# Performance work log

Hardware: AMD Instinct MI355X
Metric: run time of the kernel (lower is better)

## Reference

```python
import jax, jax.numpy as jnp
import numpy as np

B, S, H, D = 4, 2048, 16, 1024  # batch, seq, heads, n_units
DK = D // H


def setup_inputs() -> dict:
    key = jax.random.key(0)
    ks = jax.random.split(key, 12)
    k_init = float(np.sqrt(1.0 / D))
    u = lambda k, shape: jax.random.uniform(k, shape, jnp.float32, -k_init, k_init)
    # causal mask, shared across batch/heads (True = attend)
    mask = jnp.broadcast_to(jnp.tril(jnp.ones((S, S), dtype=bool)), (B, S, S))
    return {
        "query": jax.random.normal(ks[0], (B, S, D), jnp.float32),
        "key": jax.random.normal(ks[1], (B, S, D), jnp.float32),
        "value": jax.random.normal(ks[2], (B, S, D), jnp.float32),
        "Wq": u(ks[3], (H, DK, D)), "bq": u(ks[4], (H, DK)),
        "Wk": u(ks[5], (H, DK, D)), "bk": u(ks[6], (H, DK)),
        "Wv": u(ks[7], (H, DK, D)), "bv": u(ks[8], (H, DK)),
        "Wp": u(ks[9], (D, D)), "bp": u(ks[10], (D,)),
        "mask": mask,
    }


def reference(query, key, value, Wq, bq, Wk, bk, Wv, bv, Wp, bp, mask):
    # per-head projections, batched over heads: [B,S,D] x [H,DK,D] -> [B,H,S,DK]
    Q = jnp.einsum('bsd,hkd->bhsk', query, Wq) + bq[None, :, None, :]
    K = jnp.einsum('bsd,hkd->bhsk', key, Wk) + bk[None, :, None, :]
    V = jnp.einsum('bsd,hkd->bhsk', value, Wv) + bv[None, :, None, :]
    scores = jnp.einsum('bhsk,bhtk->bhst', Q, K) / jnp.sqrt(jnp.float32(DK))
    scores = jnp.where(mask[:, None, :, :], scores, jnp.float32(-1e9))
    attn = jax.nn.softmax(scores, axis=-1)  # dropout disabled (eval)
    Z = jnp.einsum('bhst,bhtk->bhsk', attn, V)
    # concat heads on feature dim: [B,S,H*DK]
    Z = jnp.transpose(Z, (0, 2, 1, 3)).reshape(B, S, D)
    return Z @ Wp.T + bp
```

## Files before the change

### kernel.cpp

```cpp
#include <hip/hip_runtime.h>

typedef __bf16 bf16;
typedef __bf16 bf16x8 __attribute__((ext_vector_type(8)));
typedef float f32x4 __attribute__((ext_vector_type(4)));

#define BB 4
#define SS 2048
#define HH 16
#define DD 1024
#define DK 64
#define MTOT (BB * SS)

#define C1 0.18033688f
#define C2 -11.5415603f

__device__ __forceinline__ void gl_lds16(const bf16* g, bf16* l)
{
    __builtin_amdgcn_global_load_lds(
        (const __attribute__((address_space(1))) unsigned int*)g,
        (__attribute__((address_space(3))) unsigned int*)l, 16, 0, 0);
}

__global__ __launch_bounds__(256) void conv_kernel(
    const float* __restrict__ q, const float* __restrict__ k,
    const float* __restrict__ v,
    const float* __restrict__ wq, const float* __restrict__ wk,
    const float* __restrict__ wv, const float* __restrict__ wp,
    bf16* __restrict__ xdst, bf16* __restrict__ wdst)
{
    const float* src; bf16* d; size_t i;
    if (blockIdx.z < 3) {
        src = (blockIdx.z == 0) ? q : (blockIdx.z == 1) ? k : v;
        d = xdst + (size_t)blockIdx.z * ((size_t)MTOT * DD);
        i = ((size_t)blockIdx.x * 256 + threadIdx.x) * 8;
    } else {
        if (blockIdx.x >= 2048) return;
        const int wsel = blockIdx.x >> 9;
        src = (wsel == 0) ? wq : (wsel == 1) ? wk : (wsel == 2) ? wv : wp;
        d = wdst + (size_t)wsel * ((size_t)DD * DD);
        i = ((size_t)(blockIdx.x & 511) * 256 + threadIdx.x) * 8;
    }
    const float4 v0 = *(const float4*)(src + i);
    const float4 v1 = *(const float4*)(src + i + 4);
    bf16x8 r = { (bf16)v0.x, (bf16)v0.y, (bf16)v0.z, (bf16)v0.w,
                 (bf16)v1.x, (bf16)v1.y, (bf16)v1.z, (bf16)v1.w };
    *(bf16x8*)(d + i) = r;
}

template<int KC, int NH>
__device__ __forceinline__ void qphase(
    const bf16* __restrict__ sb, int wm, int wn, int lr, int swz8,
    bf16x8 a[8], f32x4 acc[8][4],
    const bf16* __restrict__ ssrc, bf16* __restrict__ sdst, bool doStage)
{
    if constexpr (NH == 0) {
        #pragma unroll
        for (int i = 0; i < 8; ++i)
            a[i] = *(const bf16x8*)&sb[KC * 8192 + (wm * 128 + i * 16 + lr) * 32 + swz8];
    }
    bf16x8 b0 = *(const bf16x8*)&sb[16384 + KC * 8192 + (wn * 64 + (NH * 2 + 0) * 16 + lr) * 32 + swz8];
    bf16x8 b1 = *(const bf16x8*)&sb[16384 + KC * 8192 + (wn * 64 + (NH * 2 + 1) * 16 + lr) * 32 + swz8];
    __builtin_amdgcn_sched_barrier(0);
    __builtin_amdgcn_s_barrier();
    asm volatile("s_waitcnt lgkmcnt(0)" ::: "memory");
    __builtin_amdgcn_sched_barrier(0);
    __builtin_amdgcn_s_setprio(1);
    #pragma unroll
    for (int i = 0; i < 8; ++i) {
        acc[i][NH * 2 + 0] = __builtin_amdgcn_mfma_f32_16x16x32_bf16(
                                 a[i], b0, acc[i][NH * 2 + 0], 0, 0, 0);
        acc[i][NH * 2 + 1] = __builtin_amdgcn_mfma_f32_16x16x32_bf16(
                                 a[i], b1, acc[i][NH * 2 + 1], 0, 0, 0);
    }
    __builtin_amdgcn_s_setprio(0);
    if (doStage) {
        gl_lds16(ssrc, sdst);
        gl_lds16(ssrc + (size_t)128 * DD, sdst + 4096);
    }
    __builtin_amdgcn_sched_barrier(0);
}

__global__ __launch_bounds__(512, 2) void gemm_qkv(
    const bf16* __restrict__ x0, const bf16* __restrict__ x1,
    const bf16* __restrict__ x2, const bf16* __restrict__ w0,
    const bf16* __restrict__ w1, const bf16* __restrict__ w2,
    const float* __restrict__ bias0, const float* __restrict__ bias1,
    const float* __restrict__ bias2,
    bf16* __restrict__ o0, bf16* __restrict__ o1, bf16* __restrict__ o2)
{
    __shared__ __align__(16) bf16 smem[2 * 32768];

    const int z = blockIdx.z;
    const bf16* A = (z == 0) ? x0 : (z == 1) ? x1 : x2;
    const bf16* W = (z == 0) ? w0 : (z == 1) ? w1 : w2;
    const float* bias = (z == 0) ? bias0 : (z == 1) ? bias1 : bias2;
    bf16* out = (z == 0) ? o0 : (z == 1) ? o1 : o2;

    const int tid  = threadIdx.x;
    const int w    = tid >> 6;
    const int lane = tid & 63;
    const int quad = lane >> 4;
    const int lr   = lane & 15;
    const int wm   = w >> 2;
    const int wn   = w & 3;

    const int m_base = blockIdx.y * 256;
    const int n_base = blockIdx.x * 256;
    const int swz8 = (quad ^ ((lr >> 1) & 3)) * 8;

    const int c0 = ((tid & 3) ^ ((tid >> 3) & 3)) * 8;
    const bf16* srcA = A + (size_t)(m_base + (tid >> 2)) * DD + c0;
    const bf16* srcB = W + (size_t)(n_base + (tid >> 2)) * DD + c0;

    f32x4 acc[8][4];
    #pragma unroll
    for (int i = 0; i < 8; ++i)
        #pragma unroll
        for (int j = 0; j < 4; ++j)
            acc[i][j] = (f32x4){0.f, 0.f, 0.f, 0.f};
    bf16x8 a[8];

    #pragma unroll
    for (int t = 0; t < 2; ++t) {
        bf16* db = smem + t * 32768;
        #pragma unroll
        for (int kc = 0; kc < 2; ++kc) {
            const bf16* sA = srcA + t * 64 + kc * 32;
            const bf16* sB = srcB + t * 64 + kc * 32;
            gl_lds16(sA,                      db + kc * 8192 + w * 512);
            gl_lds16(sA + (size_t)128 * DD,   db + kc * 8192 + 4096 + w * 512);
            gl_lds16(sB,                      db + 16384 + kc * 8192 + w * 512);
            gl_lds16(sB + (size_t)128 * DD,   db + 16384 + kc * 8192 + 4096 + w * 512);
        }
    }
    asm volatile("s_waitcnt vmcnt(8)" ::: "memory");
    __builtin_amdgcn_s_barrier();

    #pragma unroll 2
    for (int T = 0; T < 16; ++T) {
        const bf16* sb = smem + (T & 1) * 32768;
        bf16* db = smem + (T & 1) * 32768;
        const bool st = (T + 2 < 16);
        const int tn = st ? (T + 2) : 0;
        const bf16* sA = srcA + tn * 64;
        const bf16* sB = srcB + tn * 64;

        qphase<0, 0>(sb, wm, wn, lr, swz8, a, acc, sA,      db + w * 512,                 st);
        __builtin_amdgcn_s_barrier();
        qphase<0, 1>(sb, wm, wn, lr, swz8, a, acc, sB,      db + 16384 + w * 512,         st);
        __builtin_amdgcn_s_barrier();
        qphase<1, 0>(sb, wm, wn, lr, swz8, a, acc, sA + 32, db + 8192 + w * 512,          st);
        __builtin_amdgcn_s_barrier();
        qphase<1, 1>(sb, wm, wn, lr, swz8, a, acc, sB + 32, db + 16384 + 8192 + w * 512,  st);
        if (st) asm volatile("s_waitcnt vmcnt(8)" ::: "memory");
        else    asm volatile("s_waitcnt vmcnt(0)" ::: "memory");
        __builtin_amdgcn_s_barrier();
    }

    if (z == 2) {
        bf16* e = smem + w * 2176;
        const int hh = (n_base + wn * 64) >> 6;
        const int mg = m_base + wm * 128;
        const int b  = mg >> 11;
        const int s0 = mg & (SS - 1);
        #pragma unroll
        for (int j = 0; j < 4; ++j) {
            const float bb = bias[n_base + wn * 64 + j * 16 + lr];
            #pragma unroll
            for (int i = 0; i < 8; ++i)
                #pragma unroll
                for (int r = 0; r < 4; ++r)
                    e[lr * 136 + i * 16 + quad * 4 + r] = (bf16)(acc[i][j][r] + bb);
            #pragma unroll
            for (int p = 0; p < 4; ++p) {
                const int nn = p * 4 + quad;
                const int mm = lr * 8;
                const bf16x8 vv = *(const bf16x8*)&e[nn * 136 + mm];
                const int dk = j * 16 + nn;
                *(bf16x8*)(out + ((size_t)(b * HH + hh) * DK + dk) * SS + s0 + mm) = vv;
            }
        }
    } else {
        #pragma unroll
        for (int j = 0; j < 4; ++j) {
            const int n  = n_base + wn * 64 + j * 16 + lr;
            const float bb = bias[n];
            const int hh = n >> 6;
            const int dk = n & (DK - 1);
            #pragma unroll
            for (int i = 0; i < 8; ++i)
                #pragma unroll
                for (int r = 0; r < 4; ++r) {
                    const int m = m_base + wm * 128 + i * 16 + quad * 4 + r;
                    const int bi = m >> 11, s = m & (SS - 1);
                    out[(((size_t)bi * HH + hh) * SS + s) * DK + dk]
                        = (bf16)(acc[i][j][r] + bb);
                }
        }
    }
}

template<int KC>
__device__ __forceinline__ void ophase(
    const bf16* __restrict__ sb, int wm, int wn, int lr, int swz8,
    f32x4 acc[4][4],
    const bf16* __restrict__ sA, const bf16* __restrict__ sB,
    bf16* __restrict__ db, int w, bool doStage)
{
    bf16x8 a[4], b[4];
    #pragma unroll
    for (int i = 0; i < 4; ++i)
        a[i] = *(const bf16x8*)&sb[KC * 8192 + (wm * 64 + i * 16 + lr) * 32 + swz8];
    #pragma unroll
    for (int j = 0; j < 4; ++j)
        b[j] = *(const bf16x8*)&sb[16384 + KC * 4096 + (wn * 64 + j * 16 + lr) * 32 + swz8];
    __builtin_amdgcn_sched_barrier(0);
    __builtin_amdgcn_s_barrier();
    asm volatile("s_waitcnt lgkmcnt(0)" ::: "memory");
    __builtin_amdgcn_sched_barrier(0);
    __builtin_amdgcn_s_setprio(1);
    #pragma unroll
    for (int i = 0; i < 4; ++i)
        #pragma unroll
        for (int j = 0; j < 4; ++j)
            acc[i][j] = __builtin_amdgcn_mfma_f32_16x16x32_bf16(
                            a[i], b[j], acc[i][j], 0, 0, 0);
    __builtin_amdgcn_s_setprio(0);
    if (doStage) {
        gl_lds16(sA + KC * 32,                    db + KC * 8192 + w * 512);
        gl_lds16(sA + KC * 32 + (size_t)128 * DD, db + KC * 8192 + 4096 + w * 512);
        gl_lds16(sB + KC * 32,                    db + 16384 + KC * 4096 + w * 512);
    }
    __builtin_amdgcn_sched_barrier(0);
}

__global__ __launch_bounds__(512, 2) void gemm_out(
    const bf16* __restrict__ A, const bf16* __restrict__ W,
    const float* __restrict__ bias, float* __restrict__ out)
{
    __shared__ __align__(16) bf16 smem[2 * 24576];

    const int tid  = threadIdx.x;
    const int w    = tid >> 6;
    const int lane = tid & 63;
    const int quad = lane >> 4;
    const int lr   = lane & 15;
    const int wm   = w >> 1;
    const int wn   = w & 1;

    const int m_base = blockIdx.y * 256;
    const int n_base = blockIdx.x * 128;
    const int swz8 = (quad ^ ((lr >> 1) & 3)) * 8;

    const int c0 = ((tid & 3) ^ ((tid >> 3) & 3)) * 8;
    const bf16* srcA = A + (size_t)(m_base + (tid >> 2)) * DD + c0;
    const bf16* srcB = W + (size_t)(n_base + (tid >> 2)) * DD + c0;

    f32x4 acc[4][4];
    #pragma unroll
    for (int i = 0; i < 4; ++i)
        #pragma unroll
        for (int j = 0; j < 4; ++j)
            acc[i][j] = (f32x4){0.f, 0.f, 0.f, 0.f};

    #pragma unroll
    for (int t = 0; t < 2; ++t) {
        bf16* db = smem + t * 24576;
        #pragma unroll
        for (int kc = 0; kc < 2; ++kc) {
            const bf16* sA = srcA + t * 64 + kc * 32;
            const bf16* sB = srcB + t * 64 + kc * 32;
            gl_lds16(sA,                      db + kc * 8192 + w * 512);
            gl_lds16(sA + (size_t)128 * DD,   db + kc * 8192 + 4096 + w * 512);
            gl_lds16(sB,                      db + 16384 + kc * 4096 + w * 512);
        }
    }
    asm volatile("s_waitcnt vmcnt(6)" ::: "memory");
    __builtin_amdgcn_s_barrier();

    #pragma unroll 2
    for (int T = 0; T < 16; ++T) {
        const bf16* sb = smem + (T & 1) * 24576;
        bf16* db = smem + (T & 1) * 24576;
        const bool st = (T + 2 < 16);
        const int tn = st ? (T + 2) : 0;
        const bf16* sA = srcA + tn * 64;
        const bf16* sB = srcB + tn * 64;

        ophase<0>(sb, wm, wn, lr, swz8, acc, sA, sB, db, w, st);
        __builtin_amdgcn_s_barrier();
        ophase<1>(sb, wm, wn, lr, swz8, acc, sA, sB, db, w, st);
        if (st) asm volatile("s_waitcnt vmcnt(6)" ::: "memory");
        else    asm volatile("s_waitcnt vmcnt(0)" ::: "memory");
        __builtin_amdgcn_s_barrier();
    }

    #pragma unroll
    for (int j = 0; j < 4; ++j) {
        const int n = n_base + wn * 64 + j * 16 + lr;
        const float bb = bias[n];
        #pragma unroll
        for (int i = 0; i < 4; ++i)
            #pragma unroll
            for (int r = 0; r < 4; ++r) {
                const int m = m_base + wm * 64 + i * 16 + quad * 4 + r;
                out[(size_t)m * DD + n] = acc[i][j][r] + bb;
            }
    }
}

template <bool DIAG>
__device__ __forceinline__ void attn_tile4(
    int quad, int lr, const bf16* __restrict__ Kc, const bf16* __restrict__ Vc,
    bf16* __restrict__ pb, const bf16x8 aq[2][2], const bf16x8& ones,
    f32x4 acc[2][4], f32x4 acc_l[2])
{
    bf16x8 kb[2][2];
    #pragma unroll
    for (int kvh = 0; kvh < 2; ++kvh)
        #pragma unroll
        for (int kc = 0; kc < 2; ++kc)
            kb[kvh][kc] = *(const bf16x8*)&Kc[
                ((kvh * 16 + lr) * 8 + ((kc * 4 + quad) ^ (lr & 7))) * 8];
    bf16x8 vb[4];
    #pragma unroll
    for (int c = 0; c < 4; ++c)
        vb[c] = *(const bf16x8*)&Vc[
            ((c * 16 + lr) * 4 + (quad ^ ((lr >> 1) & 3))) * 8];

    f32x4 s[2][2];
    #pragma unroll
    for (int h = 0; h < 2; ++h)
        #pragma unroll
        for (int kvh = 0; kvh < 2; ++kvh) {
            s[h][kvh] = (f32x4){0.f, 0.f, 0.f, 0.f};
            s[h][kvh] = __builtin_amdgcn_mfma_f32_16x16x32_bf16(
                            aq[h][0], kb[kvh][0], s[h][kvh], 0, 0, 0);
            s[h][kvh] = __builtin_amdgcn_mfma_f32_16x16x32_bf16(
                            aq[h][1], kb[kvh][1], s[h][kvh], 0, 0, 0);
        }

    #pragma unroll
    for (int h = 0; h < 2; ++h)
        #pragma unroll
        for (int kvh = 0; kvh < 2; ++kvh)
            #pragma unroll
            for (int r = 0; r < 4; ++r) {
                float p = exp2f(fmaf(s[h][kvh][r], C1, C2));
                if constexpr (DIAG) {
                    const bool ok = (kvh * 16 + lr) <= (h * 16 + quad * 4 + r);
                    p = ok ? p : 0.0f;
                }
                pb[(h * 16 + quad * 4 + r) * 40 + kvh * 16 + lr] = (bf16)p;
            }

    bf16x8 ap[2];
    #pragma unroll
    for (int h = 0; h < 2; ++h)
        ap[h] = *(const bf16x8*)&pb[(h * 16 + lr) * 40 + quad * 8];

    #pragma unroll
    for (int h = 0; h < 2; ++h)
        acc_l[h] = __builtin_amdgcn_mfma_f32_16x16x32_bf16(
                        ap[h], ones, acc_l[h], 0, 0, 0);
    #pragma unroll
    for (int c = 0; c < 4; ++c)
        #pragma unroll
        for (int h = 0; h < 2; ++h)
            acc[h][c] = __builtin_amdgcn_mfma_f32_16x16x32_bf16(
                            ap[h], vb[c], acc[h][c], 0, 0, 0);
}

__global__ __launch_bounds__(256, 4) void attn_kernel4(
    const bf16* __restrict__ q_ws, const bf16* __restrict__ k_ws,
    const bf16* __restrict__ v_ws, bf16* __restrict__ z_ws)
{
    __shared__ __align__(16) bf16 Kst[2][32 * 64];
    __shared__ __align__(16) bf16 Vst[2][64 * 32];
    __shared__ __align__(16) bf16 pbuf[4][32 * 40];

    const int tid  = threadIdx.x;
    const int w    = tid >> 6;
    const int lane = tid & 63;
    const int quad = lane >> 4;
    const int lr   = lane & 15;

    const int bh = blockIdx.x & 63;
    const int qg = 15 - (blockIdx.x >> 6);
    const int m0 = qg * 128 + w * 32;
    const int lim = 4 * qg + w;
    const int ntiles = 4 * qg + 4;

    const size_t base = (size_t)bh * SS * DK;
    const bf16* Kb = k_ws + base;
    const bf16* Vb = v_ws + base;
    bf16* pb = pbuf[w];

    const int krow = w * 8 + (lane >> 3);
    const int kcc  = (lane & 7) ^ ((lane >> 3) & 7);
    const bf16* ksrc = Kb + (size_t)krow * DK + kcc * 8;
    const int vrow = w * 16 + (lane >> 2);
    const int vcc  = (lane & 3) ^ ((lane >> 3) & 3);
    const bf16* vsrc = Vb + (size_t)vrow * SS + vcc * 8;

    bf16x8 aq[2][2];
    #pragma unroll
    for (int h = 0; h < 2; ++h)
        #pragma unroll
        for (int kc = 0; kc < 2; ++kc)
            aq[h][kc] = *(const bf16x8*)(q_ws + base
                + (size_t)(m0 + h * 16 + lr) * DK + kc * 32 + quad * 8);

    bf16x8 ones;
    #pragma unroll
    for (int i = 0; i < 8; ++i) ones[i] = (bf16)1.0f;

    f32x4 acc[2][4], acc_l[2];
    #pragma unroll
    for (int h = 0; h < 2; ++h) {
        acc_l[h] = (f32x4){0.f, 0.f, 0.f, 0.f};
        #pragma unroll
        for (int c = 0; c < 4; ++c) acc[h][c] = (f32x4){0.f, 0.f, 0.f, 0.f};
    }

    gl_lds16(ksrc, &Kst[0][w * 512]);
    gl_lds16(vsrc, &Vst[0][w * 512]);
    __syncthreads();

    for (int t = 0; t < ntiles; ++t) {
        if (t + 1 < ntiles) {
            gl_lds16(ksrc + (size_t)(t + 1) * 32 * DK, &Kst[(t + 1) & 1][w * 512]);
            gl_lds16(vsrc + (t + 1) * 32,              &Vst[(t + 1) & 1][w * 512]);
        }
        const bf16* Kc = Kst[t & 1];
        const bf16* Vc = Vst[t & 1];
        if (t < lim)
            attn_tile4<false>(quad, lr, Kc, Vc, pb, aq, ones, acc, acc_l);
        else if (t == lim)
            attn_tile4<true>(quad, lr, Kc, Vc, pb, aq, ones, acc, acc_l);
        __syncthreads();
    }

    const int b = bh >> 4, hh = bh & (HH - 1);
    #pragma unroll
    for (int h = 0; h < 2; ++h)
        #pragma unroll
        for (int r = 0; r < 4; ++r) {
            const float inv = 1.0f / acc_l[h][r];
            const int s = m0 + h * 16 + quad * 4 + r;
            #pragma unroll
            for (int c = 0; c < 4; ++c)
                z_ws[((size_t)(b * SS + s)) * DD + hh * DK + c * 16 + lr]
                    = (bf16)(acc[h][c][r] * inv);
        }
}

extern "C" void kernel_launch(void* const* d_in, const int* in_sizes, int n_in,
                              void* d_out, int out_size, void* d_ws, size_t ws_size,
                              hipStream_t stream)
{
    const float* query = (const float*)d_in[0];
    const float* key_  = (const float*)d_in[1];
    const float* value = (const float*)d_in[2];
    const float* Wq = (const float*)d_in[3];
    const float* bq = (const float*)d_in[4];
    const float* Wk = (const float*)d_in[5];
    const float* bk = (const float*)d_in[6];
    const float* Wv = (const float*)d_in[7];
    const float* bv = (const float*)d_in[8];
    const float* Wp = (const float*)d_in[9];
    const float* bp = (const float*)d_in[10];

    const size_t X = (size_t)MTOT * DD;
    const size_t W = (size_t)DD * DD;
    bf16* xq  = (bf16*)d_ws;
    bf16* xk  = xq + X;
    bf16* xv  = xk + X;
    bf16* wqb = xv + X;
    bf16* wkb = wqb + W;
    bf16* wvb = wkb + W;
    bf16* wpb = wvb + W;
    bf16* q_ws = wpb + W;
    bf16* k_ws = q_ws + X;
    bf16* v_ws = k_ws + X;
    bf16* z_ws = xq;

    conv_kernel<<<dim3(4096, 1, 4), 256, 0, stream>>>(
        query, key_, value, Wq, Wk, Wv, Wp, xq, wqb);

    gemm_qkv<<<dim3(4, 32, 3), 512, 0, stream>>>(
        xq, xk, xv, wqb, wkb, wvb, bq, bk, bv, q_ws, k_ws, v_ws);

    attn_kernel4<<<dim3(1024), 256, 0, stream>>>(q_ws, k_ws, v_ws, z_ws);

    gemm_out<<<dim3(8, 32), 512, 0, stream>>>(z_ws, wpb, bp, (float*)d_out);
}
```

Before: 355.8 us.

## Software-pipeline LDS fragment loads one phase ahead in QKV GEMM

Restructures the QKV projection GEMM main loop so that LDS reads of A/B fragments for the next phase (and the next K tile) are issued before the MFMAs of the current phase. It uses double register sets (a0/a1, b01/b23), which removes the lgkmcnt(0) wait that sat directly before each MFMA group. The global-to-LDS staging order and vmcnt thresholds are adjusted to match. This costs more VGPRs and carries some risk from the changed barrier and wait placement under the 512x2 launch bound.

After: 528.7 us. +48.6%, slower.

```diff
diff --git a/kernel.cpp b/kernel.cpp
--- a/kernel.cpp
+++ b/kernel.cpp
@@ -13,6 +13,8 @@
 
 #define C1 0.18033688f
 #define C2 -11.5415603f
+
+#define MFMA16 __builtin_amdgcn_mfma_f32_16x16x32_bf16
 
 __device__ __forceinline__ void gl_lds16(const bf16* g, bf16* l)
 {
@@ -47,39 +49,6 @@
     *(bf16x8*)(d + i) = r;
 }
 
-template<int KC, int NH>
-__device__ __forceinline__ void qphase(
-    const bf16* __restrict__ sb, int wm, int wn, int lr, int swz8,
-    bf16x8 a[8], f32x4 acc[8][4],
-    const bf16* __restrict__ ssrc, bf16* __restrict__ sdst, bool doStage)
-{
-    if constexpr (NH == 0) {
-        #pragma unroll
-        for (int i = 0; i < 8; ++i)
-            a[i] = *(const bf16x8*)&sb[KC * 8192 + (wm * 128 + i * 16 + lr) * 32 + swz8];
-    }
-    bf16x8 b0 = *(const bf16x8*)&sb[16384 + KC * 8192 + (wn * 64 + (NH * 2 + 0) * 16 + lr) * 32 + swz8];
-    bf16x8 b1 = *(const bf16x8*)&sb[16384 + KC * 8192 + (wn * 64 + (NH * 2 + 1) * 16 + lr) * 32 + swz8];
-    __builtin_amdgcn_sched_barrier(0);
-    __builtin_amdgcn_s_barrier();
-    asm volatile("s_waitcnt lgkmcnt(0)" ::: "memory");
-    __builtin_amdgcn_sched_barrier(0);
-    __builtin_amdgcn_s_setprio(1);
-    #pragma unroll
-    for (int i = 0; i < 8; ++i) {
-        acc[i][NH * 2 + 0] = __builtin_amdgcn_mfma_f32_16x16x32_bf16(
-                                 a[i], b0, acc[i][NH * 2 + 0], 0, 0, 0);
-        acc[i][NH * 2 + 1] = __builtin_amdgcn_mfma_f32_16x16x32_bf16(
-                                 a[i], b1, acc[i][NH * 2 + 1], 0, 0, 0);
-    }
-    __builtin_amdgcn_s_setprio(0);
-    if (doStage) {
-        gl_lds16(ssrc, sdst);
-        gl_lds16(ssrc + (size_t)128 * DD, sdst + 4096);
-    }
-    __builtin_amdgcn_sched_barrier(0);
-}
-
 __global__ __launch_bounds__(512, 2) void gemm_qkv(
     const bf16* __restrict__ x0, const bf16* __restrict__ x1,
     const bf16* __restrict__ x2, const bf16* __restrict__ w0,
@@ -108,6 +77,9 @@
     const int n_base = blockIdx.x * 256;
     const int swz8 = (quad ^ ((lr >> 1) & 3)) * 8;
 
+    const int ra = (wm * 128 + lr) * 32 + swz8;
+    const int rb = 16384 + (wn * 64 + lr) * 32 + swz8;
+
     const int c0 = ((tid & 3) ^ ((tid >> 3) & 3)) * 8;
     const bf16* srcA = A + (size_t)(m_base + (tid >> 2)) * DD + c0;
     const bf16* srcB = W + (size_t)(n_base + (tid >> 2)) * DD + c0;
@@ -118,42 +90,135 @@
         #pragma unroll
         for (int j = 0; j < 4; ++j)
             acc[i][j] = (f32x4){0.f, 0.f, 0.f, 0.f};
-    bf16x8 a[8];
+
+    bf16x8 a0[8], a1[8], b01[2], b23[2];
 
     #pragma unroll
     for (int t = 0; t < 2; ++t) {
         bf16* db = smem + t * 32768;
         #pragma unroll
         for (int kc = 0; kc < 2; ++kc) {
-            const bf16* sA = srcA + t * 64 + kc * 32;
-            const bf16* sB = srcB + t * 64 + kc * 32;
-            gl_lds16(sA,                      db + kc * 8192 + w * 512);
-            gl_lds16(sA + (size_t)128 * DD,   db + kc * 8192 + 4096 + w * 512);
-            gl_lds16(sB,                      db + 16384 + kc * 8192 + w * 512);
-            gl_lds16(sB + (size_t)128 * DD,   db + 16384 + kc * 8192 + 4096 + w * 512);
+            const bf16* pA = srcA + t * 64 + kc * 32;
+            const bf16* pB = srcB + t * 64 + kc * 32;
+            gl_lds16(pA,                      db + kc * 8192 + w * 512);
+            gl_lds16(pA + (size_t)128 * DD,   db + kc * 8192 + 4096 + w * 512);
+            gl_lds16(pB,                      db + 16384 + kc * 8192 + w * 512);
+            gl_lds16(pB + (size_t)128 * DD,   db + 16384 + kc * 8192 + 4096 + w * 512);
         }
     }
     asm volatile("s_waitcnt vmcnt(8)" ::: "memory");
     __builtin_amdgcn_s_barrier();
+
+    #pragma unroll
+    for (int i = 0; i < 8; ++i)
+        a0[i] = *(const bf16x8*)&smem[ra + i * 512];
+    #pragma unroll
+    for (int j = 0; j < 2; ++j)
+        b01[j] = *(const bf16x8*)&smem[rb + j * 512];
 
     #pragma unroll 2
     for (int T = 0; T < 16; ++T) {
         const bf16* sb = smem + (T & 1) * 32768;
+        const bf16* nb = smem + ((T + 1) & 1) * 32768;
         bf16* db = smem + (T & 1) * 32768;
         const bool st = (T + 2 < 16);
+        const bool nx = (T + 1 < 16);
         const int tn = st ? (T + 2) : 0;
-        const bf16* sA = srcA + tn * 64;
-        const bf16* sB = srcB + tn * 64;
-
-        qphase<0, 0>(sb, wm, wn, lr, swz8, a, acc, sA,      db + w * 512,                 st);
-        __builtin_amdgcn_s_barrier();
-        qphase<0, 1>(sb, wm, wn, lr, swz8, a, acc, sB,      db + 16384 + w * 512,         st);
-        __builtin_amdgcn_s_barrier();
-        qphase<1, 0>(sb, wm, wn, lr, swz8, a, acc, sA + 32, db + 8192 + w * 512,          st);
-        __builtin_amdgcn_s_barrier();
-        qphase<1, 1>(sb, wm, wn, lr, swz8, a, acc, sB + 32, db + 16384 + 8192 + w * 512,  st);
-        if (st) asm volatile("s_waitcnt vmcnt(8)" ::: "memory");
+        const bf16* sA = srcA + (size_t)tn * 64;
+        const bf16* sB = srcB + (size_t)tn * 64;
+
+        #pragma unroll
+        for (int j = 0; j < 2; ++j)
+            b23[j] = *(const bf16x8*)&sb[rb + (32 + j * 16) * 32];
+        #pragma unroll
+        for (int i = 0; i < 4; ++i)
+            a1[i] = *(const bf16x8*)&sb[8192 + ra + i * 512];
+        __builtin_amdgcn_sched_barrier(0);
+        __builtin_amdgcn_s_barrier();
+        __builtin_amdgcn_s_setprio(1);
+        #pragma unroll
+        for (int i = 0; i < 8; ++i) {
+            acc[i][0] = MFMA16(a0[i], b01[0], acc[i][0], 0, 0, 0);
+            acc[i][1] = MFMA16(a0[i], b01[1], acc[i][1], 0, 0, 0);
+        }
+        __builtin_amdgcn_s_setprio(0);
+        if (st) {
+            gl_lds16(sA,                    db + w * 512);
+            gl_lds16(sA + (size_t)128 * DD, db + 4096 + w * 512);
+        }
+        __builtin_amdgcn_sched_barrier(0);
+        __builtin_amdgcn_s_barrier();
+
+        #pragma unroll
+        for (int i = 4; i < 8; ++i)
+            a1[i] = *(const bf16x8*)&sb[8192 + ra + i * 512];
+        #pragma unroll
+        for (int j = 0; j < 2; ++j)
+            b01[j] = *(const bf16x8*)&sb[8192 + rb + j * 512];
+        __builtin_amdgcn_sched_barrier(0);
+        __builtin_amdgcn_s_barrier();
+        __builtin_amdgcn_s_setprio(1);
+        #pragma unroll
+        for (int i = 0; i < 8; ++i) {
+            acc[i][2] = MFMA16(a0[i], b23[0], acc[i][2], 0, 0, 0);
+            acc[i][3] = MFMA16(a0[i], b23[1], acc[i][3], 0, 0, 0);
+        }
+        __builtin_amdgcn_s_setprio(0);
+        if (st) {
+            gl_lds16(sB,                    db + 16384 + w * 512);
+            gl_lds16(sB + (size_t)128 * DD, db + 16384 + 4096 + w * 512);
+        }
+        __builtin_amdgcn_sched_barrier(0);
+        __builtin_amdgcn_s_barrier();
+
+        if (st) asm volatile("s_waitcnt vmcnt(4)" ::: "memory");
         else    asm volatile("s_waitcnt vmcnt(0)" ::: "memory");
+        if (nx) {
+            #pragma unroll
+            for (int i = 0; i < 4; ++i)
+                a0[i] = *(const bf16x8*)&nb[ra + i * 512];
+        }
+        #pragma unroll
+        for (int j = 0; j < 2; ++j)
+            b23[j] = *(const bf16x8*)&sb[8192 + rb + (32 + j * 16) * 32];
+        __builtin_amdgcn_sched_barrier(0);
+        __builtin_amdgcn_s_barrier();
+        __builtin_amdgcn_s_setprio(1);
+        #pragma unroll
+        for (int i = 0; i < 8; ++i) {
+            acc[i][0] = MFMA16(a1[i], b01[0], acc[i][0], 0, 0, 0);
+            acc[i][1] = MFMA16(a1[i], b01[1], acc[i][1], 0, 0, 0);
+        }
+        __builtin_amdgcn_s_setprio(0);
+        if (st) {
+            gl_lds16(sA + 32,                    db + 8192 + w * 512);
+            gl_lds16(sA + 32 + (size_t)128 * DD, db + 8192 + 4096 + w * 512);
+        }
+        __builtin_amdgcn_sched_barrier(0);
+        __builtin_amdgcn_s_barrier();
+
+        if (nx) {
+            #pragma unroll
+            for (int i = 4; i < 8; ++i)
+                a0[i] = *(const bf16x8*)&nb[ra + i * 512];
+            #pragma unroll
+            for (int j = 0; j < 2; ++j)
+                b01[j] = *(const bf16x8*)&nb[rb + j * 512];
+        }
+        __builtin_amdgcn_sched_barrier(0);
+        __builtin_amdgcn_s_barrier();
+        __builtin_amdgcn_s_setprio(1);
+        #pragma unroll
+        for (int i = 0; i < 8; ++i) {
+            acc[i][2] = MFMA16(a1[i], b23[0], acc[i][2], 0, 0, 0);
+            acc[i][3] = MFMA16(a1[i], b23[1], acc[i][3], 0, 0, 0);
+        }
+        __builtin_amdgcn_s_setprio(0);
+        if (st) {
+            gl_lds16(sB + 32,                    db + 16384 + 8192 + w * 512);
+            gl_lds16(sB + 32 + (size_t)128 * DD, db + 16384 + 8192 + 4096 + w * 512);
+        }
+        __builtin_amdgcn_sched_barrier(0);
         __builtin_amdgcn_s_barrier();
     }
 
```

## Retile QKV GEMM to 256x128 blocks with register double-buffered LDS pipeline

Applied to the files above, without the earlier changes.

The QKV projection GEMM moves from 256x256 to 256x128 output tiles, launches twice as many blocks, and uses a 4x2 warp layout with 64x64 per-warp tiles. The main loop now prefetches the next k-chunk's fragments into a second register set while MFMAs run, with fewer barriers per iteration and a smaller LDS footprint. The aim is better CU occupancy and a better wave count on the GPU, plus better overlap of LDS reads with compute. The cost is lower arithmetic intensity per block, since the A tile is now loaded twice as often, and the z==2 transposed epilogue had to be reworked.

Result: no change. 358.0 us (+0.6%).

```diff
diff --git a/kernel.cpp b/kernel.cpp
--- a/kernel.cpp
+++ b/kernel.cpp
@@ -13,6 +13,8 @@
 
 #define C1 0.18033688f
 #define C2 -11.5415603f
+
+#define MFMA16 __builtin_amdgcn_mfma_f32_16x16x32_bf16
 
 __device__ __forceinline__ void gl_lds16(const bf16* g, bf16* l)
 {
@@ -47,37 +49,39 @@
     *(bf16x8*)(d + i) = r;
 }
 
-template<int KC, int NH>
-__device__ __forceinline__ void qphase(
-    const bf16* __restrict__ sb, int wm, int wn, int lr, int swz8,
-    bf16x8 a[8], f32x4 acc[8][4],
-    const bf16* __restrict__ ssrc, bf16* __restrict__ sdst, bool doStage)
-{
-    if constexpr (NH == 0) {
-        #pragma unroll
-        for (int i = 0; i < 8; ++i)
-            a[i] = *(const bf16x8*)&sb[KC * 8192 + (wm * 128 + i * 16 + lr) * 32 + swz8];
-    }
-    bf16x8 b0 = *(const bf16x8*)&sb[16384 + KC * 8192 + (wn * 64 + (NH * 2 + 0) * 16 + lr) * 32 + swz8];
-    bf16x8 b1 = *(const bf16x8*)&sb[16384 + KC * 8192 + (wn * 64 + (NH * 2 + 1) * 16 + lr) * 32 + swz8];
-    __builtin_amdgcn_sched_barrier(0);
-    __builtin_amdgcn_s_barrier();
-    asm volatile("s_waitcnt lgkmcnt(0)" ::: "memory");
-    __builtin_amdgcn_sched_barrier(0);
+__device__ __forceinline__ void qkv_read_bank(
+    const bf16* __restrict__ sb, int kc, int ra, int rb,
+    bf16x8 a[4], bf16x8 b[4])
+{
+    #pragma unroll
+    for (int i = 0; i < 4; ++i)
+        a[i] = *(const bf16x8*)&sb[kc * 8192 + ra + i * 512];
+    #pragma unroll
+    for (int j = 0; j < 4; ++j)
+        b[j] = *(const bf16x8*)&sb[16384 + kc * 4096 + rb + j * 512];
+}
+
+__device__ __forceinline__ void qkv_mfma(
+    f32x4 acc[4][4], const bf16x8 a[4], const bf16x8 b[4])
+{
     __builtin_amdgcn_s_setprio(1);
     #pragma unroll
-    for (int i = 0; i < 8; ++i) {
-        acc[i][NH * 2 + 0] = __builtin_amdgcn_mfma_f32_16x16x32_bf16(
-                                 a[i], b0, acc[i][NH * 2 + 0], 0, 0, 0);
-        acc[i][NH * 2 + 1] = __builtin_amdgcn_mfma_f32_16x16x32_bf16(
-                                 a[i], b1, acc[i][NH * 2 + 1], 0, 0, 0);
-    }
+    for (int i = 0; i < 4; ++i)
+        #pragma unroll
+        for (int j = 0; j < 4; ++j)
+            acc[i][j] = MFMA16(a[i], b[j], acc[i][j], 0, 0, 0);
     __builtin_amdgcn_s_setprio(0);
-    if (doStage) {
-        gl_lds16(ssrc, sdst);
-        gl_lds16(ssrc + (size_t)128 * DD, sdst + 4096);
-    }
-    __builtin_amdgcn_sched_barrier(0);
+}
+
+__device__ __forceinline__ void qkv_stage3(
+    const bf16* __restrict__ srcA, const bf16* __restrict__ srcB,
+    bf16* __restrict__ db, int X, int kc, int w)
+{
+    const bf16* sA = srcA + X * 64 + kc * 32;
+    const bf16* sB = srcB + X * 64 + kc * 32;
+    gl_lds16(sA,                    db + kc * 8192 + w * 512);
+    gl_lds16(sA + (size_t)128 * DD, db + kc * 8192 + 4096 + w * 512);
+    gl_lds16(sB,                    db + 16384 + kc * 4096 + w * 512);
 }
 
 __global__ __launch_bounds__(512, 2) void gemm_qkv(
@@ -88,7 +92,7 @@
     const float* __restrict__ bias2,
     bf16* __restrict__ o0, bf16* __restrict__ o1, bf16* __restrict__ o2)
 {
-    __shared__ __align__(16) bf16 smem[2 * 32768];
+    __shared__ __align__(16) bf16 smem[2 * 24576];
 
     const int z = blockIdx.z;
     const bf16* A = (z == 0) ? x0 : (z == 1) ? x1 : x2;
@@ -101,83 +105,87 @@
     const int lane = tid & 63;
     const int quad = lane >> 4;
     const int lr   = lane & 15;
-    const int wm   = w >> 2;
-    const int wn   = w & 3;
+    const int wm   = w >> 1;
+    const int wn   = w & 1;
 
     const int m_base = blockIdx.y * 256;
-    const int n_base = blockIdx.x * 256;
+    const int n_base = blockIdx.x * 128;
     const int swz8 = (quad ^ ((lr >> 1) & 3)) * 8;
+
+    const int ra = (wm * 64 + lr) * 32 + swz8;
+    const int rb = (wn * 64 + lr) * 32 + swz8;
 
     const int c0 = ((tid & 3) ^ ((tid >> 3) & 3)) * 8;
     const bf16* srcA = A + (size_t)(m_base + (tid >> 2)) * DD + c0;
     const bf16* srcB = W + (size_t)(n_base + (tid >> 2)) * DD + c0;
 
-    f32x4 acc[8][4];
-    #pragma unroll
-    for (int i = 0; i < 8; ++i)
+    f32x4 acc[4][4];
+    #pragma unroll
+    for (int i = 0; i < 4; ++i)
         #pragma unroll
         for (int j = 0; j < 4; ++j)
             acc[i][j] = (f32x4){0.f, 0.f, 0.f, 0.f};
-    bf16x8 a[8];
-
-    #pragma unroll
-    for (int t = 0; t < 2; ++t) {
-        bf16* db = smem + t * 32768;
-        #pragma unroll
-        for (int kc = 0; kc < 2; ++kc) {
-            const bf16* sA = srcA + t * 64 + kc * 32;
-            const bf16* sB = srcB + t * 64 + kc * 32;
-            gl_lds16(sA,                      db + kc * 8192 + w * 512);
-            gl_lds16(sA + (size_t)128 * DD,   db + kc * 8192 + 4096 + w * 512);
-            gl_lds16(sB,                      db + 16384 + kc * 8192 + w * 512);
-            gl_lds16(sB + (size_t)128 * DD,   db + 16384 + kc * 8192 + 4096 + w * 512);
-        }
-    }
-    asm volatile("s_waitcnt vmcnt(8)" ::: "memory");
+
+    bf16x8 a0[4], b0[4], a1[4], b1[4];
+
+    qkv_stage3(srcA, srcB, smem,         0, 0, w);
+    qkv_stage3(srcA, srcB, smem,         0, 1, w);
+    qkv_stage3(srcA, srcB, smem + 24576, 1, 0, w);
+    asm volatile("s_waitcnt vmcnt(6)" ::: "memory");
     __builtin_amdgcn_s_barrier();
-
-    #pragma unroll 2
+    __builtin_amdgcn_sched_barrier(0);
+    qkv_read_bank(smem, 0, ra, rb, a0, b0);
+
     for (int T = 0; T < 16; ++T) {
-        const bf16* sb = smem + (T & 1) * 32768;
-        bf16* db = smem + (T & 1) * 32768;
-        const bool st = (T + 2 < 16);
-        const int tn = st ? (T + 2) : 0;
-        const bf16* sA = srcA + tn * 64;
-        const bf16* sB = srcB + tn * 64;
-
-        qphase<0, 0>(sb, wm, wn, lr, swz8, a, acc, sA,      db + w * 512,                 st);
+        bf16* cb = smem + (T & 1) * 24576;
+        bf16* nb = smem + ((T + 1) & 1) * 24576;
+
+        qkv_mfma(acc, a0, b0);
+        if (T < 15) {
+            qkv_stage3(srcA, srcB, nb, T + 1, 1, w);
+            asm volatile("s_waitcnt vmcnt(6)" ::: "memory");
+        } else {
+            asm volatile("s_waitcnt vmcnt(0)" ::: "memory");
+        }
+        __builtin_amdgcn_sched_barrier(0);
         __builtin_amdgcn_s_barrier();
-        qphase<0, 1>(sb, wm, wn, lr, swz8, a, acc, sB,      db + 16384 + w * 512,         st);
-        __builtin_amdgcn_s_barrier();
-        qphase<1, 0>(sb, wm, wn, lr, swz8, a, acc, sA + 32, db + 8192 + w * 512,          st);
-        __builtin_amdgcn_s_barrier();
-        qphase<1, 1>(sb, wm, wn, lr, swz8, a, acc, sB + 32, db + 16384 + 8192 + w * 512,  st);
-        if (st) asm volatile("s_waitcnt vmcnt(8)" ::: "memory");
-        else    asm volatile("s_waitcnt vmcnt(0)" ::: "memory");
-        __builtin_amdgcn_s_barrier();
+        __builtin_amdgcn_sched_barrier(0);
+        qkv_read_bank(cb, 1, ra, rb, a1, b1);
+
+        qkv_mfma(acc, a1, b1);
+        if (T <= 13)
+            qkv_stage3(srcA, srcB, cb, T + 2, 0, w);
+        if (T < 15) {
+            if (T <= 13) asm volatile("s_waitcnt vmcnt(6)" ::: "memory");
+            else         asm volatile("s_waitcnt vmcnt(3)" ::: "memory");
+            __builtin_amdgcn_sched_barrier(0);
+            __builtin_amdgcn_s_barrier();
+            __builtin_amdgcn_sched_barrier(0);
+            qkv_read_bank(nb, 0, ra, rb, a0, b0);
+        }
     }
 
     if (z == 2) {
-        bf16* e = smem + w * 2176;
-        const int hh = (n_base + wn * 64) >> 6;
-        const int mg = m_base + wm * 128;
+        bf16* e = smem + w * 1216;
+        const int h  = (blockIdx.x << 1) + wn;
+        const int mg = m_base + wm * 64;
         const int b  = mg >> 11;
         const int s0 = mg & (SS - 1);
         #pragma unroll
         for (int j = 0; j < 4; ++j) {
             const float bb = bias[n_base + wn * 64 + j * 16 + lr];
             #pragma unroll
-            for (int i = 0; i < 8; ++i)
+            for (int i = 0; i < 4; ++i)
                 #pragma unroll
                 for (int r = 0; r < 4; ++r)
-                    e[lr * 136 + i * 16 + quad * 4 + r] = (bf16)(acc[i][j][r] + bb);
+                    e[lr * 76 + i * 16 + quad * 4 + r] = (bf16)(acc[i][j][r] + bb);
             #pragma unroll
-            for (int p = 0; p < 4; ++p) {
-                const int nn = p * 4 + quad;
-                const int mm = lr * 8;
-                const bf16x8 vv = *(const bf16x8*)&e[nn * 136 + mm];
+            for (int p = 0; p < 2; ++p) {
+                const int nn = p * 8 + (lane >> 3);
+                const int mm = (lane & 7) * 8;
+                const bf16x8 vv = *(const bf16x8*)&e[nn * 76 + mm];
                 const int dk = j * 16 + nn;
-                *(bf16x8*)(out + ((size_t)(b * HH + hh) * DK + dk) * SS + s0 + mm) = vv;
+                *(bf16x8*)(out + ((size_t)(b * HH + h) * DK + dk) * SS + s0 + mm) = vv;
             }
         }
     } else {
@@ -188,10 +196,10 @@
             const int hh = n >> 6;
             const int dk = n & (DK - 1);
             #pragma unroll
-            for (int i = 0; i < 8; ++i)
+            for (int i = 0; i < 4; ++i)
                 #pragma unroll
                 for (int r = 0; r < 4; ++r) {
-                    const int m = m_base + wm * 128 + i * 16 + quad * 4 + r;
+                    const int m = m_base + wm * 64 + i * 16 + quad * 4 + r;
                     const int bi = m >> 11, s = m & (SS - 1);
                     out[(((size_t)bi * HH + hh) * SS + s) * DK + dk]
                         = (bf16)(acc[i][j][r] + bb);
@@ -488,7 +496,7 @@
     conv_kernel<<<dim3(4096, 1, 4), 256, 0, stream>>>(
         query, key_, value, Wq, Wk, Wv, Wp, xq, wqb);
 
-    gemm_qkv<<<dim3(4, 32, 3), 512, 0, stream>>>(
+    gemm_qkv<<<dim3(8, 32, 3), 512, 0, stream>>>(
         xq, xk, xv, wqb, wkb, wvb, bq, bk, bv, q_ws, k_ws, v_ws);
 
     attn_kernel4<<<dim3(1024), 256, 0, stream>>>(q_ws, k_ws, v_ws, z_ws);
```
